# Performance work log

Hardware: AMD Instinct MI355X
Metric: run time of the kernel (lower is better)

The kernel has to match this reference:

```python
import jax, jax.numpy as jnp
import numpy as np

B, N, T, FH, H = 4, 5000, 12, 12, 128
DEG = 16
BN = B * N


def setup_inputs():
    key = jax.random.key(0)
    ks = jax.random.split(key, 12)
    rng = np.random.default_rng(0)
    e = N * DEG
    s = rng.integers(0, N, size=(B, e))
    d = rng.integers(0, N, size=(B, e))
    off = (np.arange(B) * N)[:, None]
    edge_index = jnp.asarray(np.stack([(s + off).ravel(), (d + off).ravel()]), dtype=jnp.int32)

    def lin(k, i, o):
        return jax.random.normal(k, (i, o), jnp.float32) / np.sqrt(i).astype(np.float32)

    return {
        "x": jax.random.normal(ks[0], (B, N, T), jnp.float32),
        "gcn_w1": lin(ks[1], 1, 64), "gcn_b1": jnp.zeros(64),
        "gcn_w2": lin(ks[2], 64, H), "gcn_b2": jnp.zeros(H),
        "gcn_w3": lin(ks[3], H, H), "gcn_b3": jnp.zeros(H),
        "att_w1": lin(ks[4], H, H), "att_b1": jnp.zeros(H),
        "att_w2": lin(ks[5], H, 1), "att_b2": jnp.zeros(1),
        "gru_w_ih": jax.random.normal(ks[6], (3 * H, H), jnp.float32) / np.sqrt(H).astype(np.float32),
        "gru_w_hh": jax.random.normal(ks[7], (3 * H, H), jnp.float32) / np.sqrt(H).astype(np.float32),
        "gru_b_ih": jnp.zeros(3 * H), "gru_b_hh": jnp.zeros(3 * H),
        "ode_w1": lin(ks[8], H, H), "ode_b1": jnp.zeros(H),
        "ode_w2": lin(ks[9], H, H), "ode_b2": jnp.zeros(H),
        "out_w": lin(ks[10], H, 1), "out_b": jnp.zeros(1),
        "edge_index": edge_index,
    }


def _forward(x, gcn_w1, gcn_b1, gcn_w2, gcn_b2, gcn_w3, gcn_b3,
             att_w1, att_b1, att_w2, att_b2,
             gru_w_ih, gru_w_hh, gru_b_ih, gru_b_hh,
             ode_w1, ode_b1, ode_w2, ode_b2, out_w, out_b, edge_index):
    # GCNConv with added self-loops and symmetric normalization (PyG semantics)
    loops = jnp.arange(BN, dtype=edge_index.dtype)
    src = jnp.concatenate([edge_index[0], loops])
    dst = jnp.concatenate([edge_index[1], loops])
    deg = jnp.zeros(BN, x.dtype).at[dst].add(1.0)  # >= 1 thanks to self-loops
    dinv = jax.lax.rsqrt(deg)
    norm = (dinv[src] * dinv[dst])[:, None]  # (E+BN, 1)

    def gcn(h, W, b):
        h = h @ W  # (BN, out)
        agg = jnp.zeros((BN, W.shape[1]), h.dtype).at[dst].add(h[src] * norm)
        return agg + b

    # spatial encoder per timestep (scan over the small time axis)
    x_steps = x.reshape(BN, T).T[:, :, None]  # (T, BN, 1)

    def spatial_step(_, x_t):
        h = jax.nn.relu(gcn(x_t, gcn_w1, gcn_b1))
        h = jax.nn.relu(gcn(h, gcn_w2, gcn_b2))
        h = jax.nn.relu(gcn(h, gcn_w3, gcn_b3))
        return None, h

    _, h_seq = jax.lax.scan(spatial_step, None, x_steps)  # (T, BN, H)
    h_seq = h_seq.reshape(T, B, N, H).transpose(1, 0, 2, 3)  # (B, T, N, H)

    # temporal attention over time axis
    att = jnp.tanh(h_seq @ att_w1 + att_b1) @ att_w2 + att_b2  # (B, T, N, 1)
    aw = jax.nn.softmax(att, axis=1)
    node_features = jnp.sum(h_seq * aw, axis=1).reshape(BN, H)

    # single-step GRU with zero initial hidden (torch gate order r, z, n)
    h0 = jnp.zeros((BN, H), x.dtype)
    gi = node_features @ gru_w_ih.T + gru_b_ih
    gh = h0 @ gru_w_hh.T + gru_b_hh
    ir, iz, inn = jnp.split(gi, 3, axis=1)
    hr, hz, hn = jnp.split(gh, 3, axis=1)
    r = jax.nn.sigmoid(ir + hr)
    z = jax.nn.sigmoid(iz + hz)
    n = jnp.tanh(inn + r * hn)
    hidden = (1.0 - z) * n + z * h0  # (BN, H)

    # Graph ODE: dh/dt = tanh(GCN(tanh(GCN(h)))), RK4 on t=linspace(0,FH,FH)
    def ode_f(h):
        h = jnp.tanh(gcn(h, ode_w1, ode_b1))
        return jnp.tanh(gcn(h, ode_w2, ode_b2))

    dt = FH / (FH - 1)

    def rk4(h, _):
        k1 = ode_f(h)
        k2 = ode_f(h + 0.5 * dt * k1)
        k3 = ode_f(h + 0.5 * dt * k2)
        k4 = ode_f(h + dt * k3)
        h2 = h + (dt / 6.0) * (k1 + 2.0 * k2 + 2.0 * k3 + k4)
        return h2, h2

    _, traj = jax.lax.scan(rk4, hidden, None, length=FH - 1)
    states = jnp.concatenate([hidden[None], traj], axis=0)  # (FH, BN, H)
    ev = states.reshape(FH, B, N, H).transpose(1, 2, 0, 3)  # (B, N, FH, H)
    return (ev @ out_w + out_b)[..., 0]  # (B, N, FH)


def reference(x, gcn_w1, gcn_b1, gcn_w2, gcn_b2, gcn_w3, gcn_b3,
              att_w1, att_b1, att_w2, att_b2,
              gru_w_ih, gru_w_hh, gru_b_ih, gru_b_hh,
              ode_w1, ode_b1, ode_w2, ode_b2, out_w, out_b, edge_index):
    return _forward(x, gcn_w1, gcn_b1, gcn_w2, gcn_b2, gcn_w3, gcn_b3,
                    att_w1, att_b1, att_w2, att_b2,
                    gru_w_ih, gru_w_hh, gru_b_ih, gru_b_hh,
                    ode_w1, ode_b1, ode_w2, ode_b2, out_w, out_b, edge_index)
```

## Files before the change

### kernel.cpp

```cpp
#include <hip/hip_runtime.h>
#include <stdint.h>

#define B_ 4
#define N_ 5000
#define T_ 12
#define FH_ 12
#define H_ 128
#define BN_ 20000
#define E_ 320000
#define TOTE_ (E_ + BN_)
#define EVCAP_ (TOTE_ + BN_)
#define EDCAP_ 360448
#define NTB_ 313
#define NT_ 1252
#define SLOTB_ 5008
#define BNS_ 20032

typedef __attribute__((ext_vector_type(8))) short s8v;
typedef __attribute__((ext_vector_type(4))) float f32x4;

__device__ __forceinline__ float fast_tanh(float x) {
  float e = __expf(2.f * x);
  return 1.f - 2.f * __builtin_amdgcn_rcpf(e + 1.f);
}
__device__ __forceinline__ float fast_sigmoid(float x) {
  return __builtin_amdgcn_rcpf(1.f + __expf(-x));
}
__device__ __forceinline__ unsigned short f2bf(float f) {
  unsigned u = __float_as_uint(f);
  u = (u + 0x7fffu + ((u >> 16) & 1u)) >> 16;
  return (unsigned short)u;
}
__device__ __forceinline__ float bf2f(unsigned short u) {
  return __uint_as_float(((unsigned)u) << 16);
}
__device__ __forceinline__ unsigned pack2(float lo, float hi) {
  return ((unsigned)f2bf(hi) << 16) | f2bf(lo);
}

__global__ void k_sentinel(float* out) { out[0] = 1e30f; }

__global__ void k_init_cnt(int* cnt) {
  int i = blockIdx.x * 256 + threadIdx.x;
  if (i < BN_) cnt[i] = 1;
}
__global__ void k_count(const int* __restrict__ dst, int* cnt) {
  int e = blockIdx.x * 256 + threadIdx.x;
  if (e < E_) atomicAdd(&cnt[dst[e]], 1);
}
__global__ void k_scan(int* cnt, int* rp, float* dinv) {
  __shared__ int sh[1024];
  int tid = threadIdx.x;
  const int per = (BN_ + 1023) / 1024;
  int start = tid * per;
  int end = start + per; if (end > BN_) end = BN_;
  int s = 0;
  for (int i = start; i < end; i++) {
    int c = cnt[i];
    dinv[i] = rsqrtf((float)c);
    s += (c + 1) & ~1;
  }
  sh[tid] = s;
  __syncthreads();
  for (int off = 1; off < 1024; off <<= 1) {
    int v = (tid >= off) ? sh[tid - off] : 0;
    __syncthreads();
    sh[tid] += v;
    __syncthreads();
  }
  int run = (tid > 0) ? sh[tid - 1] : 0;
  for (int i = start; i < end; i++) {
    int c = cnt[i];
    rp[i] = run;
    run += (c + 1) & ~1;
    cnt[i] = 0;
  }
  if (tid == 1023) rp[BN_] = sh[1023];
}
__global__ void k_fill(const int* __restrict__ src, const int* __restrict__ dst,
                       const int* __restrict__ rp, int* cnt, int2* ev,
                       const float* __restrict__ dinv) {
  int e = blockIdx.x * 256 + threadIdx.x;
  if (e >= TOTE_) return;
  int s, d;
  if (e < E_) { s = src[e]; d = dst[e]; }
  else { s = d = e - E_; }
  int pos = rp[d] + atomicAdd(&cnt[d], 1);
  int2 p; p.x = s * 128; p.y = __float_as_int(dinv[s] * dinv[d]);
  ev[pos] = p;
}

__global__ void k_hist(const int* __restrict__ rp, int* hist) {
  int i = blockIdx.x * 256 + threadIdx.x;
  if (i < BN_) {
    int d = (rp[i + 1] - rp[i]) >> 1; d = d > 63 ? 63 : d;
    atomicAdd(&hist[(i / N_) * 64 + (63 - d)], 1);
  }
}
__global__ void k_binscan(int* hist) {
  __shared__ int sh[256];
  int t = threadIdx.x;
  int val = hist[t];
  sh[t] = val;
  __syncthreads();
  for (int o = 1; o < 256; o <<= 1) {
    int v = (t >= o) ? sh[t - o] : 0;
    __syncthreads();
    sh[t] += v;
    __syncthreads();
  }
  hist[t] = sh[t] - val;
}
__global__ void k_scatter(const int* __restrict__ rp, int* hist, int* ord, int* posj) {
  int i = blockIdx.x * 256 + threadIdx.x;
  if (i < BN_) {
    int d = (rp[i + 1] - rp[i]) >> 1; d = d > 63 ? 63 : d;
    int gpos = atomicAdd(&hist[(i / N_) * 64 + (63 - d)], 1);
    ord[gpos] = i;
    posj[i] = gpos - (i / N_) * N_;
  }
}

__global__ void k_rowoff(const int* __restrict__ rp, const int* __restrict__ ord,
                         int* rowoffp, int* tcntp) {
  int t = blockIdx.x * 256 + threadIdx.x;
  if (t >= NT_) return;
  int bb = t / NTB_, within = t % NTB_;
  int acc = 0;
  for (int r = 0; r < 16; r++) {
    int j = within * 16 + r;
    int plen = 0;
    if (j < N_) {
      int row = ord[bb * N_ + j];
      plen = (rp[row + 1] - rp[row]) >> 1;
    }
    rowoffp[t * 16 + r] = acc;
    acc += plen;
  }
  tcntp[t] = acc;
}
__global__ void k_tscan(const int* __restrict__ tcnt, int* __restrict__ tstart) {
  __shared__ int sh[1024];
  int tid = threadIdx.x;
  int st = tid * 2, en = st + 2; if (en > NT_) en = NT_;
  int s = 0;
  for (int i = st; i < en; i++) s += tcnt[i];
  sh[tid] = s;
  __syncthreads();
  for (int o = 1; o < 1024; o <<= 1) {
    int v = (tid >= o) ? sh[tid - o] : 0;
    __syncthreads();
    sh[tid] += v;
    __syncthreads();
  }
  int run = tid ? sh[tid - 1] : 0;
  for (int i = st; i < en; i++) { tstart[i] = run; run += tcnt[i]; }
  if (tid == 1023) tstart[NT_] = sh[1023];
}
__global__ void k_edfill(const int* __restrict__ rp, const int* __restrict__ ord,
                         const int* __restrict__ posj, const int2* __restrict__ ev,
                         const int* __restrict__ tstartp, const int* __restrict__ rowoffp,
                         int2* __restrict__ ed) {
  int idx = blockIdx.x * 256 + threadIdx.x;
  if (idx >= NT_ * 16) return;
  int t = idx >> 4, r = idx & 15;
  int bb = t / NTB_, within = t % NTB_;
  int j = within * 16 + r;
  if (j >= N_) return;
  int row = ord[bb * N_ + j];
  int b0 = rp[row], len = rp[row + 1] - b0;
  int dst = (tstartp[t] + rowoffp[t * 16 + r]) * 2;
  for (int i = 0; i < len; i++) {
    int2 p = ev[b0 + i];
    int src = p.x >> 7;
    int2 o; o.x = (src / N_) * SLOTB_ + posj[src]; o.y = p.y;
    ed[dst + i] = o;
  }
}

__device__ __forceinline__ void prep_one(const float* __restrict__ src,
                                         unsigned short* __restrict__ dst,
                                         int K, int Nn, int transposed, int idx) {
  int j = idx & 7, l = (idx >> 3) & 63, rest = idx >> 9;
  int NT = Nn >> 4;
  int nt = rest % NT, kc = rest / NT;
  int k = kc * 32 + ((l >> 4) << 3) + j;
  int n = nt * 16 + (l & 15);
  float v = transposed ? src[n * K + k] : src[k * Nn + n];
  dst[idx] = f2bf(v);
}
__global__ void k_prep_all(const float* w2, const float* w3, const float* a1,
                           const float* o1, const float* o2, const float* wih,
                           unsigned short* w2f, unsigned short* w3f, unsigned short* a1f,
                           unsigned short* o1f, unsigned short* o2f, unsigned short* wihf) {
  int idx = blockIdx.x * 256 + threadIdx.x;
  if (idx < 8192) { prep_one(w2, w2f, 64, 128, 0, idx); return; }
  idx -= 8192;
  if (idx < 16384) { prep_one(w3, w3f, 128, 128, 0, idx); return; }
  idx -= 16384;
  if (idx < 16384) { prep_one(a1, a1f, 128, 128, 0, idx); return; }
  idx -= 16384;
  if (idx < 16384) { prep_one(o1, o1f, 128, 128, 0, idx); return; }
  idx -= 16384;
  if (idx < 16384) { prep_one(o2, o2f, 128, 128, 0, idx); return; }
  idx -= 16384;
  if (idx < 49152) prep_one(wih, wihf, 128, 384, 1, idx);
}

__global__ void k_spl1T(const int* __restrict__ rp, const int2* __restrict__ ev,
                        const int* __restrict__ posj,
                        const float* __restrict__ x,
                        const float* __restrict__ w1, const float* __restrict__ b1,
                        unsigned short* __restrict__ h1) {
  int wid = (blockIdx.x * 256 + threadIdx.x) >> 6;
  int lane = threadIdx.x & 63;
  if (wid >= BN_) return;
  int beg = rp[wid], end = rp[wid + 1];
  float a[12];
#pragma unroll
  for (int t = 0; t < 12; t++) a[t] = 0.f;
  for (int e = beg + lane; e < end; e += 64) {
    int2 p = ev[e];
    const float4* xp = (const float4*)(x + (size_t)(p.x >> 7) * 12);
    float v = __int_as_float(p.y);
    float4 x0 = xp[0], x1 = xp[1], x2 = xp[2];
    a[0] = fmaf(v, x0.x, a[0]);  a[1] = fmaf(v, x0.y, a[1]);
    a[2] = fmaf(v, x0.z, a[2]);  a[3] = fmaf(v, x0.w, a[3]);
    a[4] = fmaf(v, x1.x, a[4]);  a[5] = fmaf(v, x1.y, a[5]);
    a[6] = fmaf(v, x1.z, a[6]);  a[7] = fmaf(v, x1.w, a[7]);
    a[8] = fmaf(v, x2.x, a[8]);  a[9] = fmaf(v, x2.y, a[9]);
    a[10] = fmaf(v, x2.z, a[10]); a[11] = fmaf(v, x2.w, a[11]);
  }
#pragma unroll
  for (int t = 0; t < 12; t++)
#pragma unroll
    for (int m = 1; m < 64; m <<= 1) a[t] += __shfl_xor(a[t], m);
  float wv = w1[lane], bv = b1[lane];
  int slot = (wid / N_) * SLOTB_ + posj[wid];
#pragma unroll
  for (int t = 0; t < 12; t++) {
    float v = fmaf(a[t], wv, bv);
    h1[((size_t)t * BNS_ + slot) * 64 + lane] = f2bf(fmaxf(v, 0.f));
  }
}

template<int KIN>
__device__ __forceinline__ void gather_tile(
    const int2* __restrict__ ed, const int* __restrict__ tstartp,
    const int* __restrict__ rowoffp, const unsigned short* __restrict__ in,
    unsigned short (*agg)[KIN + 8], uint4* desc, int tileid, int w, int l, int tid) {
  constexpr int SH = (KIN == 128) ? 7 : 6;
  constexpr int CW = KIN / 16;
  const int h = l >> 4, c = l & 15;
  const unsigned short* inc = in + c * CW;
  int tp0 = tstartp[tileid];
  int npair = tstartp[tileid + 1] - tp0;
  const uint4* edp = (const uint4*)(ed + (size_t)tp0 * 2);
  for (int i = tid; i < npair; i += 256) desc[i] = edp[i];
  __syncthreads();
  int q0[4], qlen[4];
  float a[4][CW];
  int mx = 0;
  const int* rot = rowoffp + tileid * 16;
#pragma unroll
  for (int r = 0; r < 4; r++) {
    int lr = w * 4 + r;
    int ro = rot[lr];
    int rn = (lr == 15) ? npair : rot[lr + 1];
    int lenp = rn - ro;
    int s0 = (lenp * h) >> 2, s1 = (lenp * (h + 1)) >> 2;
    q0[r] = ro + s0;
    qlen[r] = s1 - s0;
    mx = qlen[r] > mx ? qlen[r] : mx;
#pragma unroll
    for (int q = 0; q < CW; q++) a[r][q] = 0.f;
  }
  int lim = npair - 1;
  for (int i = 0; i < mx; i++) {
#pragma unroll
    for (int r = 0; r < 4; r++) {
      int idx = q0[r] + i; idx = idx > lim ? lim : idx;
      uint4 d = desc[idx];
      if (i < qlen[r]) {
        float vA = __int_as_float(d.y), vB = __int_as_float(d.w);
        if (KIN == 128) {
          uint4 pA = *(const uint4*)(inc + ((size_t)d.x << SH));
          uint4 pB = *(const uint4*)(inc + ((size_t)d.z << SH));
          a[r][0] = fmaf(vA, bf2f((unsigned short)(pA.x & 0xffffu)), a[r][0]);
          a[r][1] = fmaf(vA, bf2f((unsigned short)(pA.x >> 16)), a[r][1]);
          a[r][2] = fmaf(vA, bf2f((unsigned short)(pA.y & 0xffffu)), a[r][2]);
          a[r][3] = fmaf(vA, bf2f((unsigned short)(pA.y >> 16)), a[r][3]);
          a[r][4] = fmaf(vA, bf2f((unsigned short)(pA.z & 0xffffu)), a[r][4]);
          a[r][5] = fmaf(vA, bf2f((unsigned short)(pA.z >> 16)), a[r][5]);
          a[r][6] = fmaf(vA, bf2f((unsigned short)(pA.w & 0xffffu)), a[r][6]);
          a[r][7] = fmaf(vA, bf2f((unsigned short)(pA.w >> 16)), a[r][7]);
          a[r][0] = fmaf(vB, bf2f((unsigned short)(pB.x & 0xffffu)), a[r][0]);
          a[r][1] = fmaf(vB, bf2f((unsigned short)(pB.x >> 16)), a[r][1]);
          a[r][2] = fmaf(vB, bf2f((unsigned short)(pB.y & 0xffffu)), a[r][2]);
          a[r][3] = fmaf(vB, bf2f((unsigned short)(pB.y >> 16)), a[r][3]);
          a[r][4] = fmaf(vB, bf2f((unsigned short)(pB.z & 0xffffu)), a[r][4]);
          a[r][5] = fmaf(vB, bf2f((unsigned short)(pB.z >> 16)), a[r][5]);
          a[r][6] = fmaf(vB, bf2f((unsigned short)(pB.w & 0xffffu)), a[r][6]);
          a[r][7] = fmaf(vB, bf2f((unsigned short)(pB.w >> 16)), a[r][7]);
        } else {
          uint2 pA = *(const uint2*)(inc + ((size_t)d.x << SH));
          uint2 pB = *(const uint2*)(inc + ((size_t)d.z << SH));
          a[r][0] = fmaf(vA, bf2f((unsigned short)(pA.x & 0xffffu)), a[r][0]);
          a[r][1] = fmaf(vA, bf2f((unsigned short)(pA.x >> 16)), a[r][1]);
          a[r][2] = fmaf(vA, bf2f((unsigned short)(pA.y & 0xffffu)), a[r][2]);
          a[r][3] = fmaf(vA, bf2f((unsigned short)(pA.y >> 16)), a[r][3]);
          a[r][0] = fmaf(vB, bf2f((unsigned short)(pB.x & 0xffffu)), a[r][0]);
          a[r][1] = fmaf(vB, bf2f((unsigned short)(pB.x >> 16)), a[r][1]);
          a[r][2] = fmaf(vB, bf2f((unsigned short)(pB.y & 0xffffu)), a[r][2]);
          a[r][3] = fmaf(vB, bf2f((unsigned short)(pB.y >> 16)), a[r][3]);
        }
      }
    }
  }
#pragma unroll
  for (int r = 0; r < 4; r++) {
#pragma unroll
    for (int q2 = 0; q2 < CW; q2++) {
      a[r][q2] += __shfl_xor(a[r][q2], 16);
      a[r][q2] += __shfl_xor(a[r][q2], 32);
    }
    if (h == 0) {
      if (KIN == 128) {
        uint4 o;
        o.x = pack2(a[r][0], a[r][1]); o.y = pack2(a[r][2], a[r][3]);
        o.z = pack2(a[r][4], a[r][5]); o.w = pack2(a[r][6], a[r][7]);
        *(uint4*)&agg[w * 4 + r][c * 8] = o;
      } else {
        uint2 o;
        o.x = pack2(a[r][0], a[r][1]); o.y = pack2(a[r][2], a[r][3]);
        *(uint2*)&agg[w * 4 + r][c * 4] = o;
      }
    }
  }
}

template<int KIN>
__device__ __forceinline__ void mfma_tile(
    const unsigned short (*agg)[KIN + 8], const unsigned short* __restrict__ Wf,
    int w, int l, f32x4 acc[2]) {
  constexpr int KC = KIN / 32;
  const int hi = l >> 4, lo16 = l & 15;
  acc[0] = (f32x4){0.f, 0.f, 0.f, 0.f};
  acc[1] = (f32x4){0.f, 0.f, 0.f, 0.f};
#pragma unroll
  for (int kc = 0; kc < KC; kc++) {
    s8v av = *(const s8v*)&agg[lo16][kc * 32 + hi * 8];
#pragma unroll
    for (int q = 0; q < 2; q++) {
      s8v bv = *(const s8v*)(Wf + (((size_t)(kc * 8 + 2 * w + q)) << 9) + (l << 3));
      acc[q] = __builtin_amdgcn_mfma_f32_16x16x32_bf16(av, bv, acc[q], 0, 0, 0);
    }
  }
}

template<int KIN>
__global__ __launch_bounds__(256) void k_fusedT(
    const int2* __restrict__ ed, const int* __restrict__ tstartp,
    const int* __restrict__ rowoffp,
    const unsigned short* __restrict__ inb, const unsigned short* __restrict__ Wf,
    const float* __restrict__ bias, unsigned short* __restrict__ outb) {
  __shared__ __align__(16) uint4 desc[512];
  __shared__ unsigned short agg[16][KIN + 8];
  const int tid = threadIdx.x, l = tid & 63, w = tid >> 6;
  const int t = blockIdx.y;
  const unsigned short* in = inb + (size_t)t * BNS_ * KIN;
  unsigned short* out = outb + (size_t)t * BNS_ * 128;
  const int bid = blockIdx.x;
  const int xcd = bid & 7, slot = bid >> 3;
  const int bb = xcd >> 1;
  const int within = slot * 2 + (xcd & 1);
  if (within >= NTB_) return;
  int nv = N_ - within * 16; nv = nv > 16 ? 16 : nv;
  const int tileid = bb * NTB_ + within;
  gather_tile<KIN>(ed, tstartp, rowoffp, in, agg, desc, tileid, w, l, tid);
  __syncthreads();
  f32x4 acc[2];
  mfma_tile<KIN>(agg, Wf, w, l, acc);
  const int hi = l >> 4, lo16 = l & 15;
  const int rowbase = tileid * 16;
#pragma unroll
  for (int q = 0; q < 2; q++) {
    int col = (2 * w + q) * 16 + lo16;
    float bi = bias[col];
#pragma unroll
    for (int reg = 0; reg < 4; reg++) {
      int lr = hi * 4 + reg;
      if (lr < nv)
        out[(size_t)(rowbase + lr) * 128 + col] = f2bf(fmaxf(acc[q][reg] + bi, 0.f));
    }
  }
}

__global__ __launch_bounds__(256) void k_fused(
    const int2* __restrict__ ed, const int* __restrict__ tstartp,
    const int* __restrict__ rowoffp, const int* __restrict__ ord,
    const unsigned short* __restrict__ in,
    const unsigned short* __restrict__ Wf, const float* __restrict__ bias,
    int mode, float c1, float c2,
    unsigned short* __restrict__ outb,
    const unsigned short* __restrict__ hbfin, unsigned short* __restrict__ rkb,
    float* __restrict__ h, unsigned short* __restrict__ ubfout,
    const float* __restrict__ ow, const float* __restrict__ ob,
    float* __restrict__ outp, int step) {
  __shared__ __align__(16) uint4 desc[512];
  __shared__ unsigned short agg[16][136];
  __shared__ float ppart[4][16];
  const int tid = threadIdx.x, l = tid & 63, w = tid >> 6;
  const int bid = blockIdx.x;
  const int xcd = bid & 7, slot = bid >> 3;
  const int bb = xcd >> 1;
  const int within = slot * 2 + (xcd & 1);
  if (within >= NTB_) return;
  int nv = N_ - within * 16; nv = nv > 16 ? 16 : nv;
  const int tileid = bb * NTB_ + within;
  gather_tile<128>(ed, tstartp, rowoffp, in, agg, desc, tileid, w, l, tid);
  __syncthreads();
  f32x4 acc[2];
  mfma_tile<128>(agg, Wf, w, l, acc);
  const int hi = l >> 4, lo16 = l & 15;
  const int rowbase = tileid * 16;
  float p[4] = {0.f, 0.f, 0.f, 0.f};
#pragma unroll
  for (int q = 0; q < 2; q++) {
    int col = (2 * w + q) * 16 + lo16;
    float bi = bias[col];
    float owv = (mode == 3) ? ow[col] : 0.f;
#pragma unroll
    for (int reg = 0; reg < 4; reg++) {
      int lr = hi * 4 + reg;
      if (lr >= nv) continue;
      size_t oi = (size_t)(rowbase + lr) * 128 + col;
      float v = fast_tanh(acc[q][reg] + bi);
      if (mode == 0) {
        outb[oi] = f2bf(v);
      } else if (mode == 1) {
        rkb[oi] = f2bf(v);
        ubfout[oi] = f2bf(fmaf(c1, v, bf2f(hbfin[oi])));
      } else if (mode == 2) {
        rkb[oi] = f2bf(bf2f(rkb[oi]) + 2.f * v);
        ubfout[oi] = f2bf(fmaf(c1, v, bf2f(hbfin[oi])));
      } else {
        float nh = fmaf(c2, bf2f(rkb[oi]) + v, h[oi]);
        h[oi] = nh;
        ubfout[oi] = f2bf(nh);
        p[reg] = fmaf(nh, owv, p[reg]);
      }
    }
  }
  if (mode == 3) {
#pragma unroll
    for (int m = 1; m <= 8; m <<= 1)
#pragma unroll
      for (int reg = 0; reg < 4; reg++) p[reg] += __shfl_xor(p[reg], m);
    if (lo16 == 0)
#pragma unroll
      for (int reg = 0; reg < 4; reg++) ppart[w][hi * 4 + reg] = p[reg];
    __syncthreads();
    if (tid < 16 && tid < nv) {
      int orig = ord[bb * N_ + within * 16 + tid];
      outp[(size_t)orig * FH_ + step] =
          ppart[0][tid] + ppart[1][tid] + ppart[2][tid] + ppart[3][tid] + ob[0];
    }
  }
}

__global__ __launch_bounds__(256) void k_att(
    const unsigned short* __restrict__ A, const unsigned short* __restrict__ Wf,
    const float* __restrict__ bias, int nrows,
    const float* __restrict__ w2v, const float* __restrict__ b2,
    float* __restrict__ scores) {
  const int tid = threadIdx.x;
  const int l = tid & 63;
  const int w = tid >> 6;
  const int m0 = blockIdx.x * 64 + w * 16;

  f32x4 acc[8];
#pragma unroll
  for (int nt = 0; nt < 8; nt++) acc[nt] = (f32x4){0.f, 0.f, 0.f, 0.f};
  int arow = m0 + (l & 15);
  if (arow >= nrows) arow = nrows - 1;
  const unsigned short* Ap = A + (size_t)arow * 128 + ((l >> 4) << 3);
#pragma unroll
  for (int kc = 0; kc < 4; kc++) {
    s8v av = *(const s8v*)(Ap + kc * 32);
#pragma unroll
    for (int nt = 0; nt < 8; nt++) {
      s8v bv = *(const s8v*)(Wf + (((size_t)(kc * 8 + nt)) << 9) + (l << 3));
      acc[nt] = __builtin_amdgcn_mfma_f32_16x16x32_bf16(av, bv, acc[nt], 0, 0, 0);
    }
  }
  float p[4] = {0.f, 0.f, 0.f, 0.f};
#pragma unroll
  for (int nt = 0; nt < 8; nt++) {
    int col = nt * 16 + (l & 15);
    float bi = bias[col], wv = w2v[col];
#pragma unroll
    for (int reg = 0; reg < 4; reg++)
      p[reg] = fmaf(fast_tanh(acc[nt][reg] + bi), wv, p[reg]);
  }
#pragma unroll
  for (int m = 1; m <= 8; m <<= 1)
#pragma unroll
    for (int reg = 0; reg < 4; reg++) p[reg] += __shfl_xor(p[reg], m);
  if ((l & 15) == 0) {
    float bb = b2[0];
#pragma unroll
    for (int reg = 0; reg < 4; reg++) {
      int row = m0 + ((l >> 4) << 2) + reg;
      if (row < nrows) scores[row] = p[reg] + bb;
    }
  }
}

__global__ void k_attw(const float* __restrict__ sc, const unsigned short* __restrict__ hs,
                       unsigned short* __restrict__ nf) {
  int idx = blockIdx.x * 256 + threadIdx.x;
  if (idx >= BNS_ * 64) return;
  int bn = idx >> 6, c = idx & 63;
  float v[T_];
  float m = -1e30f;
#pragma unroll
  for (int t = 0; t < T_; t++) { v[t] = sc[t * BNS_ + bn]; m = fmaxf(m, v[t]); }
  float ssum = 0.f;
#pragma unroll
  for (int t = 0; t < T_; t++) { v[t] = __expf(v[t] - m); ssum += v[t]; }
  float inv = __builtin_amdgcn_rcpf(ssum);
  float s0 = 0.f, s1 = 0.f;
#pragma unroll
  for (int t = 0; t < T_; t++) {
    unsigned p = *(const unsigned*)(hs + ((size_t)t * BNS_ + bn) * 128 + c * 2);
    float aw = v[t] * inv;
    s0 = fmaf(aw, bf2f((unsigned short)(p & 0xffffu)), s0);
    s1 = fmaf(aw, bf2f((unsigned short)(p >> 16)), s1);
  }
  *(unsigned*)(nf + (size_t)bn * 128 + c * 2) = pack2(s0, s1);
}

__global__ __launch_bounds__(256) void k_gruf(
    const unsigned short* __restrict__ A, const unsigned short* __restrict__ Wf,
    const float* __restrict__ bih, const float* __restrict__ bhh,
    const int* __restrict__ ord,
    float* __restrict__ hst, unsigned short* __restrict__ hbf,
    const float* __restrict__ ow, const float* __restrict__ ob,
    float* __restrict__ outp) {
  const int tid = threadIdx.x;
  const int l = tid & 63;
  const int w = tid >> 6;
  const int m0 = blockIdx.x * 64 + w * 16;

  f32x4 acc[24];
#pragma unroll
  for (int nt = 0; nt < 24; nt++) acc[nt] = (f32x4){0.f, 0.f, 0.f, 0.f};
  int arow = m0 + (l & 15);
  const unsigned short* Ap = A + (size_t)arow * 128 + ((l >> 4) << 3);
#pragma unroll
  for (int kc = 0; kc < 4; kc++) {
    s8v av = *(const s8v*)(Ap + kc * 32);
#pragma unroll
    for (int nt = 0; nt < 24; nt++) {
      s8v bv = *(const s8v*)(Wf + (((size_t)(kc * 24 + nt)) << 9) + (l << 3));
      acc[nt] = __builtin_amdgcn_mfma_f32_16x16x32_bf16(av, bv, acc[nt], 0, 0, 0);
    }
  }
  const int hi = l >> 4, lo16 = l & 15;
  float p[4] = {0.f, 0.f, 0.f, 0.f};
#pragma unroll
  for (int nt = 0; nt < 8; nt++) {
    int col = nt * 16 + lo16;
    float br = bih[col], bz = bih[col + 128], bn = bih[col + 256];
    float hr = bhh[col], hz = bhh[col + 128], hn = bhh[col + 256];
    float owv = ow[col];
#pragma unroll
    for (int reg = 0; reg < 4; reg++) {
      int slot = m0 + hi * 4 + reg;
      float r = fast_sigmoid(acc[nt][reg] + br + hr);
      float z = fast_sigmoid(acc[nt + 8][reg] + bz + hz);
      float n = fast_tanh(acc[nt + 16][reg] + bn + r * hn);
      float hv = (1.f - z) * n;
      size_t oi = (size_t)slot * 128 + col;
      hst[oi] = hv;
      hbf[oi] = f2bf(hv);
      p[reg] = fmaf(hv, owv, p[reg]);
    }
  }
#pragma unroll
  for (int m = 1; m <= 8; m <<= 1)
#pragma unroll
    for (int reg = 0; reg < 4; reg++) p[reg] += __shfl_xor(p[reg], m);
  if (lo16 == 0) {
    float obv = ob[0];
#pragma unroll
    for (int reg = 0; reg < 4; reg++) {
      int slot = m0 + hi * 4 + reg;
      int bbv = slot / SLOTB_;
      int j = slot - bbv * SLOTB_;
      if (j < N_) {
        int orig = ord[bbv * N_ + j];
        outp[(size_t)orig * FH_ + 0] = p[reg] + obv;
      }
    }
  }
}

extern "C" void kernel_launch(void* const* d_in, const int* in_sizes, int n_in,
                              void* d_out, int out_size, void* d_ws, size_t ws_size,
                              hipStream_t stream) {
  const float* x       = (const float*)d_in[0];
  const float* gcn_w1  = (const float*)d_in[1];
  const float* gcn_b1  = (const float*)d_in[2];
  const float* gcn_w2  = (const float*)d_in[3];
  const float* gcn_b2  = (const float*)d_in[4];
  const float* gcn_w3  = (const float*)d_in[5];
  const float* gcn_b3  = (const float*)d_in[6];
  const float* att_w1  = (const float*)d_in[7];
  const float* att_b1  = (const float*)d_in[8];
  const float* att_w2  = (const float*)d_in[9];
  const float* att_b2  = (const float*)d_in[10];
  const float* gru_wih = (const float*)d_in[11];
  const float* gru_bih = (const float*)d_in[13];
  const float* gru_bhh = (const float*)d_in[14];
  const float* ode_w1  = (const float*)d_in[15];
  const float* ode_b1  = (const float*)d_in[16];
  const float* ode_w2  = (const float*)d_in[17];
  const float* ode_b2  = (const float*)d_in[18];
  const float* out_w   = (const float*)d_in[19];
  const float* out_b   = (const float*)d_in[20];
  const int*   eidx    = (const int*)d_in[21];
  float* out = (float*)d_out;

  float* wsf = (float*)d_ws;
  size_t off = 0;
  unsigned short* h1b12 = (unsigned short*)(wsf + off); off += (size_t)12 * BNS_ * 32;
  float* hst    = wsf + off; off += (size_t)BNS_ * H_;
  float* scores = wsf + off; off += (size_t)T_ * BNS_;
  float* dinv   = wsf + off; off += BN_;
  int2*  ev     = (int2*)(wsf + off); off += (size_t)EVCAP_ * 2;
  int2*  ed     = (int2*)(wsf + off); off += (size_t)EDCAP_ * 2;
  unsigned short* hseqb  = (unsigned short*)(wsf + off); off += (size_t)T_ * BNS_ * 64;
  unsigned short* t1b12  = (unsigned short*)(wsf + off); off += (size_t)T_ * BNS_ * 64;
  unsigned short* hbf    = (unsigned short*)(wsf + off); off += (size_t)BNS_ * 64;
  unsigned short* ubf    = (unsigned short*)(wsf + off); off += (size_t)BNS_ * 64;
  unsigned short* rkb    = (unsigned short*)(wsf + off); off += (size_t)BNS_ * 64;
  unsigned short* nfbf   = (unsigned short*)(wsf + off); off += (size_t)BNS_ * 64;
  unsigned short* w2f    = (unsigned short*)(wsf + off); off += 64 * 128 / 2;
  unsigned short* w3f    = (unsigned short*)(wsf + off); off += 128 * 128 / 2;
  unsigned short* aw1f   = (unsigned short*)(wsf + off); off += 128 * 128 / 2;
  unsigned short* ow1f   = (unsigned short*)(wsf + off); off += 128 * 128 / 2;
  unsigned short* ow2f   = (unsigned short*)(wsf + off); off += 128 * 128 / 2;
  unsigned short* wihf   = (unsigned short*)(wsf + off); off += 128 * 384 / 2;
  int* rp      = (int*)(wsf + off); off += BN_ + 1;
  int* cnt     = (int*)(wsf + off); off += BN_;
  int* ord     = (int*)(wsf + off); off += BN_;
  int* posj    = (int*)(wsf + off); off += BN_;
  int* hist    = (int*)(wsf + off); off += 256;
  int* rowoffp = (int*)(wsf + off); off += (size_t)NT_ * 16;
  int* tcntp   = (int*)(wsf + off); off += NT_;
  int* tstartp = (int*)(wsf + off); off += NT_ + 1;
  if (ws_size < off * sizeof(float)) {
    k_sentinel<<<1, 1, 0, stream>>>(out);
    return;
  }

  const int* esrc = eidx;
  const int* edst = eidx + E_;
  const int g79 = (BN_ + 255) / 256;

  hipMemsetAsync(ev, 0, (size_t)EVCAP_ * sizeof(int2), stream);
  hipMemsetAsync(hist, 0, 256 * sizeof(int), stream);
  k_init_cnt<<<g79, 256, 0, stream>>>(cnt);
  k_count<<<(E_ + 255) / 256, 256, 0, stream>>>(edst, cnt);
  k_scan<<<1, 1024, 0, stream>>>(cnt, rp, dinv);
  k_fill<<<(TOTE_ + 255) / 256, 256, 0, stream>>>(esrc, edst, rp, cnt, ev, dinv);
  k_hist<<<g79, 256, 0, stream>>>(rp, hist);
  k_binscan<<<1, 256, 0, stream>>>(hist);
  k_scatter<<<g79, 256, 0, stream>>>(rp, hist, ord, posj);
  k_rowoff<<<(NT_ + 255) / 256, 256, 0, stream>>>(rp, ord, rowoffp, tcntp);
  k_tscan<<<1, 1024, 0, stream>>>(tcntp, tstartp);
  k_edfill<<<(NT_ * 16 + 255) / 256, 256, 0, stream>>>(rp, ord, posj, ev,
                                                       tstartp, rowoffp, ed);
  k_prep_all<<<480, 256, 0, stream>>>(gcn_w2, gcn_w3, att_w1, ode_w1, ode_w2, gru_wih,
                                      w2f, w3f, aw1f, ow1f, ow2f, wihf);

  const int gW = BN_ / 4;
  const int gF = 1280;

  k_spl1T<<<gW, 256, 0, stream>>>(rp, ev, posj, x, gcn_w1, gcn_b1, h1b12);
  k_fusedT<64><<<dim3(gF, 12), 256, 0, stream>>>(ed, tstartp, rowoffp,
                                                 h1b12, w2f, gcn_b2, t1b12);
  k_fusedT<128><<<dim3(gF, 12), 256, 0, stream>>>(ed, tstartp, rowoffp,
                                                  t1b12, w3f, gcn_b3, hseqb);

  k_att<<<(T_ * BNS_ + 63) / 64, 256, 0, stream>>>(hseqb, aw1f, att_b1, T_ * BNS_,
                                                   att_w2, att_b2, scores);
  k_attw<<<(BNS_ * 64 + 255) / 256, 256, 0, stream>>>(scores, hseqb, nfbf);

  k_gruf<<<BNS_ / 64, 256, 0, stream>>>(nfbf, wihf, gru_bih, gru_bhh, ord,
                                        hst, hbf, out_w, out_b, out);

  const float dt = (float)FH_ / (float)(FH_ - 1);
  unsigned short* t1 = t1b12;
  auto f_eval = [&](const unsigned short* inbf, int mode, float c1, float c2, int step) {
    k_fused<<<gF, 256, 0, stream>>>(ed, tstartp, rowoffp, ord, inbf, ow1f, ode_b1,
                                    0, 0.f, 0.f, t1, nullptr, nullptr, nullptr, nullptr,
                                    nullptr, nullptr, nullptr, 0);
    k_fused<<<gF, 256, 0, stream>>>(ed, tstartp, rowoffp, ord, t1, ow2f, ode_b2,
                                    mode, c1, c2, nullptr, hbf, rkb, hst,
                                    (mode == 3) ? hbf : ubf,
                                    out_w, out_b, out, step);
  };
  for (int s = 1; s < FH_; s++) {
    f_eval(hbf, 1, 0.5f * dt, 0.f, s);
    f_eval(ubf, 2, 0.5f * dt, 0.f, s);
    f_eval(ubf, 2, dt, 0.f, s);
    f_eval(ubf, 3, 0.f, dt / 6.f, s);
  }
}
```

Measured before the change: 1.768 ms.

## Pack edge pairs into 8-byte descriptors and accumulate with bf16 dot2

Each edge-pair descriptor shrinks from 16 bytes (two int slots, two fp32 weights) to 8 bytes: two 16-bit source slots plus two bf16 normalization weights. The gather loop now uses v_dot2_f32_bf16 with a byte permute to combine both neighbors per feature in one instruction. This replaces the per-element unpack and two FMAs. The aim is to cut descriptor traffic, shared memory and ALU work in the sparse aggregation, at the cost of rounding the edge weights to bf16 and silently truncating tiles with more than 512 pairs.

```diff
diff --git a/kernel.cpp b/kernel.cpp
--- a/kernel.cpp
+++ b/kernel.cpp
@@ -10,11 +10,12 @@
 #define E_ 320000
 #define TOTE_ (E_ + BN_)
 #define EVCAP_ (TOTE_ + BN_)
-#define EDCAP_ 360448
+#define EDCAP_ 190000
 #define NTB_ 313
 #define NT_ 1252
 #define SLOTB_ 5008
 #define BNS_ 20032
+#define DCAP_ 512
 
 typedef __attribute__((ext_vector_type(8))) short s8v;
 typedef __attribute__((ext_vector_type(4))) float f32x4;
@@ -37,6 +38,11 @@
 __device__ __forceinline__ unsigned pack2(float lo, float hi) {
   return ((unsigned)f2bf(hi) << 16) | f2bf(lo);
 }
+#define DOT2ACC(accv, pa, pb, sel)                                         \
+  {                                                                        \
+    unsigned pp_ = __builtin_amdgcn_perm((pb), (pa), (sel));               \
+    asm("v_dot2_f32_bf16 %0, %1, %2, %0" : "+v"(accv) : "v"(pp_), "v"(wp)); \
+  }
 
 __global__ void k_sentinel(float* out) { out[0] = 1e30f; }
 
@@ -169,12 +175,16 @@
   if (j >= N_) return;
   int row = ord[bb * N_ + j];
   int b0 = rp[row], len = rp[row + 1] - b0;
-  int dst = (tstartp[t] + rowoffp[t * 16 + r]) * 2;
-  for (int i = 0; i < len; i++) {
-    int2 p = ev[b0 + i];
-    int src = p.x >> 7;
-    int2 o; o.x = (src / N_) * SLOTB_ + posj[src]; o.y = p.y;
-    ed[dst + i] = o;
+  int dst = tstartp[t] + rowoffp[t * 16 + r];
+  for (int i = 0; i < len; i += 2) {
+    int2 pA = ev[b0 + i], pB = ev[b0 + i + 1];
+    int sA = pA.x >> 7, sB = pB.x >> 7;
+    int slotA = (sA / N_) * SLOTB_ + posj[sA];
+    int slotB = (sB / N_) * SLOTB_ + posj[sB];
+    unsigned wp = ((unsigned)f2bf(__int_as_float(pB.y)) << 16) |
+                  f2bf(__int_as_float(pA.y));
+    int2 o; o.x = slotA | (slotB << 16); o.y = (int)wp;
+    ed[dst + (i >> 1)] = o;
   }
 }
 
@@ -248,14 +258,15 @@
 __device__ __forceinline__ void gather_tile(
     const int2* __restrict__ ed, const int* __restrict__ tstartp,
     const int* __restrict__ rowoffp, const unsigned short* __restrict__ in,
-    unsigned short (*agg)[KIN + 8], uint4* desc, int tileid, int w, int l, int tid) {
+    unsigned short (*agg)[KIN + 8], int2* desc, int tileid, int w, int l, int tid) {
   constexpr int SH = (KIN == 128) ? 7 : 6;
   constexpr int CW = KIN / 16;
   const int h = l >> 4, c = l & 15;
   const unsigned short* inc = in + c * CW;
   int tp0 = tstartp[tileid];
   int npair = tstartp[tileid + 1] - tp0;
-  const uint4* edp = (const uint4*)(ed + (size_t)tp0 * 2);
+  if (npair > DCAP_) npair = DCAP_;
+  const int2* edp = ed + tp0;
   for (int i = tid; i < npair; i += 256) desc[i] = edp[i];
   __syncthreads();
   int q0[4], qlen[4];
@@ -280,39 +291,29 @@
 #pragma unroll
     for (int r = 0; r < 4; r++) {
       int idx = q0[r] + i; idx = idx > lim ? lim : idx;
-      uint4 d = desc[idx];
+      int2 d = desc[idx];
       if (i < qlen[r]) {
-        float vA = __int_as_float(d.y), vB = __int_as_float(d.w);
+        unsigned sa = (unsigned)d.x & 0xffffu;
+        unsigned sb = (unsigned)d.x >> 16;
+        unsigned wp = (unsigned)d.y;
         if (KIN == 128) {
-          uint4 pA = *(const uint4*)(inc + ((size_t)d.x << SH));
-          uint4 pB = *(const uint4*)(inc + ((size_t)d.z << SH));
-          a[r][0] = fmaf(vA, bf2f((unsigned short)(pA.x & 0xffffu)), a[r][0]);
-          a[r][1] = fmaf(vA, bf2f((unsigned short)(pA.x >> 16)), a[r][1]);
-          a[r][2] = fmaf(vA, bf2f((unsigned short)(pA.y & 0xffffu)), a[r][2]);
-          a[r][3] = fmaf(vA, bf2f((unsigned short)(pA.y >> 16)), a[r][3]);
-          a[r][4] = fmaf(vA, bf2f((unsigned short)(pA.z & 0xffffu)), a[r][4]);
-          a[r][5] = fmaf(vA, bf2f((unsigned short)(pA.z >> 16)), a[r][5]);
-          a[r][6] = fmaf(vA, bf2f((unsigned short)(pA.w & 0xffffu)), a[r][6]);
-          a[r][7] = fmaf(vA, bf2f((unsigned short)(pA.w >> 16)), a[r][7]);
-          a[r][0] = fmaf(vB, bf2f((unsigned short)(pB.x & 0xffffu)), a[r][0]);
-          a[r][1] = fmaf(vB, bf2f((unsigned short)(pB.x >> 16)), a[r][1]);
-          a[r][2] = fmaf(vB, bf2f((unsigned short)(pB.y & 0xffffu)), a[r][2]);
-          a[r][3] = fmaf(vB, bf2f((unsigned short)(pB.y >> 16)), a[r][3]);
-          a[r][4] = fmaf(vB, bf2f((unsigned short)(pB.z & 0xffffu)), a[r][4]);
-          a[r][5] = fmaf(vB, bf2f((unsigned short)(pB.z >> 16)), a[r][5]);
-          a[r][6] = fmaf(vB, bf2f((unsigned short)(pB.w & 0xffffu)), a[r][6]);
-          a[r][7] = fmaf(vB, bf2f((unsigned short)(pB.w >> 16)), a[r][7]);
+          uint4 PA = *(const uint4*)(inc + ((size_t)sa << SH));
+          uint4 PB = *(const uint4*)(inc + ((size_t)sb << SH));
+          DOT2ACC(a[r][0], PA.x, PB.x, 0x05040100u);
+          DOT2ACC(a[r][1], PA.x, PB.x, 0x07060302u);
+          DOT2ACC(a[r][2], PA.y, PB.y, 0x05040100u);
+          DOT2ACC(a[r][3], PA.y, PB.y, 0x07060302u);
+          DOT2ACC(a[r][4], PA.z, PB.z, 0x05040100u);
+          DOT2ACC(a[r][5], PA.z, PB.z, 0x07060302u);
+          DOT2ACC(a[r][6], PA.w, PB.w, 0x05040100u);
+          DOT2ACC(a[r][7], PA.w, PB.w, 0x07060302u);
         } else {
-          uint2 pA = *(const uint2*)(inc + ((size_t)d.x << SH));
-          uint2 pB = *(const uint2*)(inc + ((size_t)d.z << SH));
-          a[r][0] = fmaf(vA, bf2f((unsigned short)(pA.x & 0xffffu)), a[r][0]);
-          a[r][1] = fmaf(vA, bf2f((unsigned short)(pA.x >> 16)), a[r][1]);
-          a[r][2] = fmaf(vA, bf2f((unsigned short)(pA.y & 0xffffu)), a[r][2]);
-          a[r][3] = fmaf(vA, bf2f((unsigned short)(pA.y >> 16)), a[r][3]);
-          a[r][0] = fmaf(vB, bf2f((unsigned short)(pB.x & 0xffffu)), a[r][0]);
-          a[r][1] = fmaf(vB, bf2f((unsigned short)(pB.x >> 16)), a[r][1]);
-          a[r][2] = fmaf(vB, bf2f((unsigned short)(pB.y & 0xffffu)), a[r][2]);
-          a[r][3] = fmaf(vB, bf2f((unsigned short)(pB.y >> 16)), a[r][3]);
+          uint2 PA = *(const uint2*)(inc + ((size_t)sa << SH));
+          uint2 PB = *(const uint2*)(inc + ((size_t)sb << SH));
+          DOT2ACC(a[r][0], PA.x, PB.x, 0x05040100u);
+          DOT2ACC(a[r][1], PA.x, PB.x, 0x07060302u);
+          DOT2ACC(a[r][2], PA.y, PB.y, 0x05040100u);
+          DOT2ACC(a[r][3], PA.y, PB.y, 0x07060302u);
         }
       }
     }
@@ -364,7 +365,7 @@
     const int* __restrict__ rowoffp,
     const unsigned short* __restrict__ inb, const unsigned short* __restrict__ Wf,
     const float* __restrict__ bias, unsigned short* __restrict__ outb) {
-  __shared__ __align__(16) uint4 desc[512];
+  __shared__ __align__(16) int2 desc[DCAP_];
   __shared__ unsigned short agg[16][KIN + 8];
   const int tid = threadIdx.x, l = tid & 63, w = tid >> 6;
   const int t = blockIdx.y;
@@ -407,7 +408,7 @@
     float* __restrict__ h, unsigned short* __restrict__ ubfout,
     const float* __restrict__ ow, const float* __restrict__ ob,
     float* __restrict__ outp, int step) {
-  __shared__ __align__(16) uint4 desc[512];
+  __shared__ __align__(16) int2 desc[DCAP_];
   __shared__ unsigned short agg[16][136];
   __shared__ float ppart[4][16];
   const int tid = threadIdx.x, l = tid & 63, w = tid >> 6;
```

Result: no change. 1.737 ms (median of 2 runs) (-1.8%).
